# Kernel optimization log

Hardware: AMD Instinct MI355X
Metric: run time of the kernel (lower is better)

## Reference

```python
import jax, jax.numpy as jnp
import numpy as np

D_MODEL = 2048
N_HEADS = 16
D_HEAD = 128
N_GROUPS = 4          # KV heads = N_HEADS // N_GROUPS = 4
D_FF = 2048           # hard-coded default in FeedForward
EPS = 1e-6


def setup_inputs() -> dict:
    key = jax.random.key(0)
    ks = jax.random.split(key, 16)
    B, S = 4, 1024
    Hkv = N_HEADS // N_GROUPS
    s = 0.02
    inp = {
        "x": jax.random.normal(ks[0], (B, S, D_MODEL), jnp.float32),
        "scale1": jnp.ones((D_MODEL,), jnp.float32),
        "Wq": jax.random.normal(ks[1], (D_MODEL, N_HEADS * D_HEAD), jnp.float32) * s,
        "bq": jnp.zeros((N_HEADS * D_HEAD,), jnp.float32),
        "Wk": jax.random.normal(ks[2], (D_MODEL, Hkv * D_HEAD), jnp.float32) * s,
        "bk": jnp.zeros((Hkv * D_HEAD,), jnp.float32),
        "Wv": jax.random.normal(ks[3], (D_MODEL, Hkv * D_HEAD), jnp.float32) * s,
        "bv": jnp.zeros((Hkv * D_HEAD,), jnp.float32),
        "Wo": jax.random.normal(ks[4], (N_HEADS * D_HEAD, D_MODEL), jnp.float32) * s,
        "bo": jnp.zeros((D_MODEL,), jnp.float32),
        "W1": jax.random.normal(ks[5], (D_MODEL, D_FF), jnp.float32) * s,
        "b1": jnp.zeros((D_FF,), jnp.float32),
        "W2": jax.random.normal(ks[6], (D_FF, D_MODEL), jnp.float32) * s,
        "b2": jnp.zeros((D_MODEL,), jnp.float32),
    }
    return inp


def _rmsnorm(x, scale):
    rms = jnp.sqrt(jnp.mean(x * x, axis=-1, keepdims=True) + EPS)
    return scale * (x / rms)


def reference(x, scale1, Wq, bq, Wk, bk, Wv, bv, Wo, bo, W1, b1, W2, b2):
    B, S, _ = x.shape
    Hkv = N_HEADS // N_GROUPS
    xn = _rmsnorm(x, scale1)  # [B,S,D]

    # GQA attention (prefill, step=None -> no cache)
    Q = (xn @ Wq + bq).reshape(B, S, N_HEADS, D_HEAD).transpose(0, 2, 1, 3)  # [B,H,S,d]
    K = (xn @ Wk + bk).reshape(B, S, Hkv, D_HEAD).transpose(0, 2, 1, 3)      # [B,Hkv,S,d]
    V = (xn @ Wv + bv).reshape(B, S, Hkv, D_HEAD).transpose(0, 2, 1, 3)
    Kr = jnp.repeat(K, N_GROUPS, axis=1)  # [B,H,S,d]
    Vr = jnp.repeat(V, N_GROUPS, axis=1)
    scores = jnp.einsum("bhqd,bhkd->bhqk", Q, Kr) / jnp.sqrt(jnp.float32(D_HEAD))
    attn = jax.nn.softmax(scores, axis=-1)
    out = jnp.einsum("bhqk,bhkd->bhqd", attn, Vr)  # [B,H,S,d]
    out = out.transpose(0, 2, 1, 3).reshape(B, S, N_HEADS * D_HEAD)
    x = x + out @ Wo + bo

    # Source bug preserved: FFN consumes rms_norm1 output, rms_norm2 is dead code
    h = xn @ W1 + b1
    h = h * jax.nn.sigmoid(h) * h  # x_ff * silu(x_ff)
    x = x + h @ W2 + b2
    return x
```

## Files before the change

kernel.cpp:

```cpp
#include <hip/hip_runtime.h>
#include <hip/hip_bf16.h>
#include <cstdint>

using bf16 = __hip_bfloat16;
typedef __attribute__((ext_vector_type(8))) __bf16 bf16x8;
typedef __attribute__((ext_vector_type(4))) float f32x4;

#define MFMA16(a, b, c) __builtin_amdgcn_mfma_f32_16x16x32_bf16((a), (b), (c), 0, 0, 0)

#if __has_builtin(__builtin_amdgcn_exp2f)
__device__ __forceinline__ float fexp2(float x) { return __builtin_amdgcn_exp2f(x); }
#else
__device__ __forceinline__ float fexp2(float x) { return exp2f(x); }
#endif

__device__ __forceinline__ void async16(void* lds_ptr, const void* gptr) {
  auto g = reinterpret_cast<__attribute__((address_space(1))) unsigned int*>(
      reinterpret_cast<uintptr_t>(gptr));
  auto l = reinterpret_cast<__attribute__((address_space(3))) unsigned int*>(
      static_cast<unsigned int>(reinterpret_cast<uintptr_t>(lds_ptr)));
  __builtin_amdgcn_global_load_lds(g, l, 16, 0, 0);
}

__global__ __launch_bounds__(256) void rmsnorm_cast_k(
    const float* __restrict__ x, const float* __restrict__ sc, bf16* __restrict__ xn) {
  const int row = blockIdx.x, tid = threadIdx.x;
  const float4* xr = (const float4*)(x + (size_t)row * 2048);
  float4 a = xr[tid * 2], b = xr[tid * 2 + 1];
  float ss = a.x * a.x + a.y * a.y + a.z * a.z + a.w * a.w +
             b.x * b.x + b.y * b.y + b.z * b.z + b.w * b.w;
#pragma unroll
  for (int d = 1; d < 64; d <<= 1) ss += __shfl_xor(ss, d);
  __shared__ float sm[4];
  if ((tid & 63) == 0) sm[tid >> 6] = ss;
  __syncthreads();
  const float rinv = rsqrtf((sm[0] + sm[1] + sm[2] + sm[3]) * (1.0f / 2048.0f) + 1e-6f);
  const float4* sp = (const float4*)sc;
  float4 s0 = sp[tid * 2], s1 = sp[tid * 2 + 1];
  union { bf16 h[8]; bf16x8 v; } o;
  o.h[0] = __float2bfloat16(a.x * rinv * s0.x);
  o.h[1] = __float2bfloat16(a.y * rinv * s0.y);
  o.h[2] = __float2bfloat16(a.z * rinv * s0.z);
  o.h[3] = __float2bfloat16(a.w * rinv * s0.w);
  o.h[4] = __float2bfloat16(b.x * rinv * s1.x);
  o.h[5] = __float2bfloat16(b.y * rinv * s1.y);
  o.h[6] = __float2bfloat16(b.z * rinv * s1.z);
  o.h[7] = __float2bfloat16(b.w * rinv * s1.w);
  *(bf16x8*)(xn + (size_t)row * 2048 + tid * 8) = o.v;
}

__global__ void transpose_cast_k(const float* __restrict__ W, bf16* __restrict__ Wt,
                                 int N, int row_off) {
  __shared__ float t[32][33];
  const int n0 = blockIdx.x * 32, k0 = blockIdx.y * 32;
  const int tx = threadIdx.x, ty = threadIdx.y;
#pragma unroll
  for (int i = 0; i < 4; ++i)
    t[ty + 8 * i][tx] = W[(size_t)(k0 + ty + 8 * i) * N + n0 + tx];
  __syncthreads();
#pragma unroll
  for (int i = 0; i < 4; ++i)
    Wt[(size_t)(row_off + n0 + ty + 8 * i) * 2048 + k0 + tx] =
        __float2bfloat16(t[tx][ty + 8 * i]);
}

__global__ void transpose_v_k(const bf16* __restrict__ qkv, bf16* __restrict__ vtb) {
  __shared__ bf16 t[32][33];
  const int bh = blockIdx.z, b = bh >> 2, g = bh & 3;
  const int s0 = blockIdx.x * 32, d0 = blockIdx.y * 32;
  const int tx = threadIdx.x, ty = threadIdx.y;
#pragma unroll
  for (int i = 0; i < 4; ++i)
    t[ty + 8 * i][tx] =
        qkv[(size_t)(b * 1024 + s0 + ty + 8 * i) * 3072 + 2560 + g * 128 + d0 + tx];
  __syncthreads();
#pragma unroll
  for (int i = 0; i < 4; ++i)
    vtb[((size_t)bh * 128 + d0 + ty + 8 * i) * 1024 + s0 + tx] = t[tx][ty + 8 * i];
}

__global__ void concat_bias_k(const float* __restrict__ bq, const float* __restrict__ bk,
                              const float* __restrict__ bv, const float* __restrict__ b1,
                              float* __restrict__ o) {
  const int i = blockIdx.x * 256 + threadIdx.x;
  if (i < 2048) o[i] = bq[i];
  else if (i < 2560) o[i] = bk[i - 2048];
  else if (i < 3072) o[i] = bv[i - 2560];
  else o[i] = b1[i - 3072];
}

#define GR_PHASE(HH, DO_STAGE, VMW)                                                \
  {                                                                                \
    const int sa = ((HH) & 3) * 8192, sb = 32768 + sa;                             \
    bf16x8 af[4], bf_[4];                                                          \
    _Pragma("unroll") for (int mi = 0; mi < 4; ++mi) {                             \
      const int R = (w >> 1) * 64 + mi * 16 + lo;                                  \
      af[mi] = *(const bf16x8*)(lds + sa + R * 64 + ((hi ^ ((R >> 1) & 3)) << 4)); \
    }                                                                              \
    _Pragma("unroll") for (int nj = 0; nj < 4; ++nj) {                             \
      const int S = (w & 1) * 64 + nj * 16 + lo;                                   \
      bf_[nj] = *(const bf16x8*)(lds + sb + S * 64 + ((hi ^ ((S >> 1) & 3)) << 4)); \
    }                                                                              \
    DO_STAGE;                                                                      \
    asm volatile("s_waitcnt vmcnt(" #VMW ")" ::: "memory");                        \
    __builtin_amdgcn_sched_barrier(0);                                             \
    __builtin_amdgcn_s_barrier();                                                  \
    asm volatile("" ::: "memory");                                                 \
    __builtin_amdgcn_s_setprio(1);                                                 \
    _Pragma("unroll") for (int mi = 0; mi < 4; ++mi)                               \
      _Pragma("unroll") for (int nj = 0; nj < 4; ++nj)                             \
        acc[mi][nj] = MFMA16(af[mi], bf_[nj], acc[mi][nj]);                        \
    __builtin_amdgcn_s_setprio(0);                                                 \
    asm volatile("" ::: "memory");                                                 \
    __builtin_amdgcn_s_barrier();                                                  \
    asm volatile("" ::: "memory");                                                 \
  }

template <int EPI>
__global__ __launch_bounds__(256, 2) void gemm_r(
    const bf16* __restrict__ A, const bf16* __restrict__ Bt,
    const float* __restrict__ bias, const float* __restrict__ res,
    void* __restrict__ out0, void* __restrict__ out1, int K) {
  __shared__ __align__(16) unsigned char lds[65536];
  const int tid = threadIdx.x, lane = tid & 63, w = tid >> 6;
  const int hi = lane >> 4, lo = lane & 15;
  const int brow = blockIdx.x * 128, bcol = blockIdx.y * 128;
  const int nt = K >> 6;

  const int o0 = tid * 16, o1 = o0 + 4096;
  const int r0 = o0 >> 6, c0 = ((((o0 >> 4) & 3) ^ ((r0 >> 1) & 3)) << 3);
  const int r1 = o1 >> 6, c1 = ((((o1 >> 4) & 3) ^ ((r1 >> 1) & 3)) << 3);
  const bf16* gA0 = A + (size_t)(brow + r0) * K + c0;
  const bf16* gA1 = A + (size_t)(brow + r1) * K + c1;
  const bf16* gB0 = Bt + (size_t)(bcol + r0) * K + c0;
  const bf16* gB1 = Bt + (size_t)(bcol + r1) * K + c1;

  auto stg = [&](int h) {
    const int s = (h & 3) * 8192;
    const int kb = h * 32;
    async16(lds + s + o0, gA0 + kb);
    async16(lds + s + o1, gA1 + kb);
    async16(lds + 32768 + s + o0, gB0 + kb);
    async16(lds + 32768 + s + o1, gB1 + kb);
  };

  stg(0); stg(1); stg(2);
  asm volatile("s_waitcnt vmcnt(8)" ::: "memory");
  __builtin_amdgcn_sched_barrier(0);
  __builtin_amdgcn_s_barrier();
  asm volatile("" ::: "memory");

  f32x4 acc[4][4] = {};
  int t = 0;
  for (; t < nt - 2; ++t) {
    GR_PHASE(2 * t,     stg(2 * t + 3), 8);
    GR_PHASE(2 * t + 1, stg(2 * t + 4), 8);
  }
  GR_PHASE(2 * t,     stg(2 * t + 3), 8);
  GR_PHASE(2 * t + 1, (void)0, 4);
  ++t;
  GR_PHASE(2 * t,     (void)0, 0);
  GR_PHASE(2 * t + 1, (void)0, 0);

#pragma unroll
  for (int nj = 0; nj < 4; ++nj) {
    const int col = bcol + (w & 1) * 64 + nj * 16 + lo;
    const float bs = bias[col];
#pragma unroll
    for (int mi = 0; mi < 4; ++mi) {
      const int row0 = brow + (w >> 1) * 64 + mi * 16 + hi * 4;
#pragma unroll
      for (int r = 0; r < 4; ++r) {
        float v = acc[mi][nj][r] + bs;
        const int row = row0 + r;
        if (EPI == 0) {
          if (bcol < 3072) {
            ((bf16*)out0)[(size_t)row * 3072 + col] = __float2bfloat16(v);
          } else {
            const float sg = 1.0f / (1.0f + __expf(-v));
            v = v * sg * v;
            ((bf16*)out1)[(size_t)row * 2048 + (col - 3072)] = __float2bfloat16(v);
          }
        } else {
          v += res[(size_t)row * 2048 + col];
          ((float*)out0)[(size_t)row * 2048 + col] = v;
        }
      }
    }
  }
}

__global__ __launch_bounds__(256, 4) void attn_fwd(
    const bf16* __restrict__ qkv, const bf16* __restrict__ vtb, bf16* __restrict__ out) {
  __shared__ __align__(16) unsigned char lds[40960];
  unsigned char* Ks = lds;
  unsigned char* Vs = lds + 16384;
  unsigned char* Ps = lds + 32768;
  const int tid = threadIdx.x, lane = tid & 63, w = tid >> 6;
  const int hi = lane >> 4, lo = lane & 15;
  const int qt = blockIdx.x, bh = blockIdx.y;
  const int b = bh >> 4, h = bh & 15, g = h >> 2;
  const size_t tok0 = (size_t)b * 1024;
  const int q0 = qt * 64;

  bf16x8 qf[4];
  {
    const bf16* qp = qkv + (tok0 + q0 + w * 16 + lo) * 3072 + h * 128 + hi * 8;
#pragma unroll
    for (int kc = 0; kc < 4; ++kc) qf[kc] = *(const bf16x8*)(qp + kc * 32);
  }

  float m2 = -1e30f, lsum = 0.f;
  f32x4 oacc[8] = {};
  const float c2 = 0.08838834764831845f * 1.44269504088896f;

  const int o = tid * 16;
  const bf16* kbase = qkv + tok0 * 3072 + 2048 + g * 128;
  const bf16* vbase = vtb + (size_t)(b * 4 + g) * 128 * 1024;
  unsigned char* Pw = Ps + w * 2048;

  for (int t = 0; t < 16; ++t) {
    const int kb = t * 64;
#pragma unroll
    for (int rd = 0; rd < 4; ++rd) {
      const int oo = o + rd * 4096;
      const int rK = oo >> 8, cK = ((oo >> 4) & 15) ^ (rK & 15);
      const int rV = oo >> 7, cV = ((oo >> 4) & 7) ^ (rV & 7);
      async16(Ks + oo, kbase + (size_t)(kb + rK) * 3072 + cK * 8);
      async16(Vs + oo, vbase + (size_t)rV * 1024 + kb + cV * 8);
    }
    __syncthreads();

    f32x4 sc[4] = {};
#pragma unroll
    for (int kc = 0; kc < 4; ++kc) {
#pragma unroll
      for (int kg = 0; kg < 4; ++kg) {
        const int row = kg * 16 + lo;
        bf16x8 kf = *(const bf16x8*)(Ks + row * 256 + ((((kc << 2) + hi) ^ (row & 15)) << 4));
        sc[kg] = MFMA16(kf, qf[kc], sc[kg]);
      }
    }

    float mx = sc[0][0];
#pragma unroll
    for (int kg = 0; kg < 4; ++kg)
#pragma unroll
      for (int r = 0; r < 4; ++r) mx = fmaxf(mx, sc[kg][r]);
    mx = fmaxf(mx, __shfl_xor(mx, 16));
    mx = fmaxf(mx, __shfl_xor(mx, 32));
    mx *= c2;
    const float mn = fmaxf(m2, mx);
    const float corr = fexp2(m2 - mn);
    m2 = mn;

    float rs = 0.f;
#pragma unroll
    for (int kg = 0; kg < 4; ++kg) {
      union { bf16 hh[4]; uint2 v; } pk;
#pragma unroll
      for (int r = 0; r < 4; ++r) {
        const float p = fexp2(sc[kg][r] * c2 - mn);
        rs += p;
        pk.hh[r] = __float2bfloat16(p);
      }
      *(uint2*)(Pw + lo * 128 + ((((kg << 1) + (hi >> 1)) ^ (lo & 7)) << 4) +
                ((hi & 1) << 3)) = pk.v;
    }
    rs += __shfl_xor(rs, 16);
    rs += __shfl_xor(rs, 32);
    lsum = lsum * corr + rs;

    float corr_r[4];
#pragma unroll
    for (int r = 0; r < 4; ++r) corr_r[r] = __shfl(corr, hi * 4 + r);
#pragma unroll
    for (int dg = 0; dg < 8; ++dg)
#pragma unroll
      for (int r = 0; r < 4; ++r) oacc[dg][r] *= corr_r[r];

    asm volatile("s_waitcnt lgkmcnt(0)" ::: "memory");

    bf16x8 pf[2];
#pragma unroll
    for (int kc = 0; kc < 2; ++kc)
      pf[kc] = *(const bf16x8*)(Pw + lo * 128 + ((((kc << 2) + hi) ^ (lo & 7)) << 4));
#pragma unroll
    for (int dg = 0; dg < 8; ++dg) {
#pragma unroll
      for (int kc = 0; kc < 2; ++kc) {
        const int vrow = dg * 16 + lo;
        bf16x8 vf = *(const bf16x8*)(Vs + vrow * 128 + ((((kc << 2) + hi) ^ (vrow & 7)) << 4));
        oacc[dg] = MFMA16(pf[kc], vf, oacc[dg]);
      }
    }
    __syncthreads();
  }

  const float linv = 1.0f / lsum;
  float lr[4];
#pragma unroll
  for (int r = 0; r < 4; ++r) lr[r] = __shfl(linv, hi * 4 + r);
  bf16* op = out + (tok0 + q0 + w * 16 + hi * 4) * 2048 + h * 128 + lo;
#pragma unroll
  for (int dg = 0; dg < 8; ++dg)
#pragma unroll
    for (int r = 0; r < 4; ++r)
      op[(size_t)r * 2048 + dg * 16] = __float2bfloat16(oacc[dg][r] * lr[r]);
}

extern "C" void kernel_launch(void* const* d_in, const int* in_sizes, int n_in,
                              void* d_out, int out_size, void* d_ws, size_t ws_size,
                              hipStream_t stream) {
  (void)in_sizes; (void)n_in; (void)out_size; (void)ws_size;
  const float* x  = (const float*)d_in[0];
  const float* s1 = (const float*)d_in[1];
  const float* Wq = (const float*)d_in[2];
  const float* bq = (const float*)d_in[3];
  const float* Wk = (const float*)d_in[4];
  const float* bk = (const float*)d_in[5];
  const float* Wv = (const float*)d_in[6];
  const float* bv = (const float*)d_in[7];
  const float* Wo = (const float*)d_in[8];
  const float* bo = (const float*)d_in[9];
  const float* W1 = (const float*)d_in[10];
  const float* b1 = (const float*)d_in[11];
  const float* W2 = (const float*)d_in[12];
  const float* b2 = (const float*)d_in[13];
  float* outp = (float*)d_out;

  char* ws = (char*)d_ws;
  bf16*  xn    = (bf16*)(ws + 0);
  bf16*  vtb   = (bf16*)(ws + 0);
  bf16*  wcatT = (bf16*)(ws + 16777216);
  bf16*  attnb = (bf16*)(ws + 16777216);
  float* bcat  = (float*)(ws + 37748736);
  bf16*  woT   = (bf16*)(ws + 37769216);
  bf16*  w2T   = (bf16*)(ws + 46157824);
  bf16*  qkvb  = (bf16*)(ws + 54546432);
  bf16*  gbuf  = (bf16*)(ws + 79712256);
  float* x1    = outp;

  const dim3 b32x8(32, 8);
  rmsnorm_cast_k<<<dim3(4096), dim3(256), 0, stream>>>(x, s1, xn);
  concat_bias_k<<<dim3(20), dim3(256), 0, stream>>>(bq, bk, bv, b1, bcat);
  transpose_cast_k<<<dim3(64, 64), b32x8, 0, stream>>>(Wq, wcatT, 2048, 0);
  transpose_cast_k<<<dim3(16, 64), b32x8, 0, stream>>>(Wk, wcatT, 512, 2048);
  transpose_cast_k<<<dim3(16, 64), b32x8, 0, stream>>>(Wv, wcatT, 512, 2560);
  transpose_cast_k<<<dim3(64, 64), b32x8, 0, stream>>>(W1, wcatT, 2048, 3072);
  transpose_cast_k<<<dim3(64, 64), b32x8, 0, stream>>>(Wo, woT, 2048, 0);
  transpose_cast_k<<<dim3(64, 64), b32x8, 0, stream>>>(W2, w2T, 2048, 0);
  gemm_r<0><<<dim3(32, 40), dim3(256), 0, stream>>>(xn, wcatT, bcat, (const float*)nullptr,
                                                    (void*)qkvb, (void*)gbuf, 2048);
  transpose_v_k<<<dim3(32, 4, 16), b32x8, 0, stream>>>(qkvb, vtb);
  attn_fwd<<<dim3(16, 64), dim3(256), 0, stream>>>(qkvb, vtb, attnb);
  gemm_r<1><<<dim3(32, 16), dim3(256), 0, stream>>>(attnb, woT, bo, x, (void*)x1,
                                                    (void*)nullptr, 2048);
  gemm_r<1><<<dim3(32, 16), dim3(256), 0, stream>>>(gbuf, w2T, b2, x1, (void*)outp,
                                                    (void*)nullptr, 2048);
}
```

Baseline: 284.4 us.

## Double-buffer LDS fragment reads and cut barriers in GEMM main loop

Restructures the GEMM inner loop so the LDS fragments for the next half-tile are read into a second register set while the current one feeds the MFMAs. This drops one of the two s_barriers per phase and deepens the global-load wait so stages are kept further ahead. It adds 32 extra VGPRs of fragment storage, which may strain occupancy at launch bound 2, and depends on subtle synchronisation correctness across the 4-slot ring.

Result: no change. 287.2 us (+1.0%).

```diff
diff --git a/kernel.cpp b/kernel.cpp
--- a/kernel.cpp
+++ b/kernel.cpp
@@ -89,32 +89,31 @@
   else o[i] = b1[i - 3072];
 }
 
-#define GR_PHASE(HH, DO_STAGE, VMW)                                                \
+#define PH_READ(AF, BF, SLOT)                                                      \
   {                                                                                \
-    const int sa = ((HH) & 3) * 8192, sb = 32768 + sa;                             \
-    bf16x8 af[4], bf_[4];                                                          \
+    const int sa = (SLOT)*8192, sb = 32768 + sa;                                   \
     _Pragma("unroll") for (int mi = 0; mi < 4; ++mi) {                             \
       const int R = (w >> 1) * 64 + mi * 16 + lo;                                  \
-      af[mi] = *(const bf16x8*)(lds + sa + R * 64 + ((hi ^ ((R >> 1) & 3)) << 4)); \
+      AF[mi] = *(const bf16x8*)(lds + sa + R * 64 + ((hi ^ ((R >> 1) & 3)) << 4)); \
     }                                                                              \
     _Pragma("unroll") for (int nj = 0; nj < 4; ++nj) {                             \
       const int S = (w & 1) * 64 + nj * 16 + lo;                                   \
-      bf_[nj] = *(const bf16x8*)(lds + sb + S * 64 + ((hi ^ ((S >> 1) & 3)) << 4)); \
+      BF[nj] = *(const bf16x8*)(lds + sb + S * 64 + ((hi ^ ((S >> 1) & 3)) << 4)); \
     }                                                                              \
-    DO_STAGE;                                                                      \
-    asm volatile("s_waitcnt vmcnt(" #VMW ")" ::: "memory");                        \
-    __builtin_amdgcn_sched_barrier(0);                                             \
-    __builtin_amdgcn_s_barrier();                                                  \
-    asm volatile("" ::: "memory");                                                 \
-    __builtin_amdgcn_s_setprio(1);                                                 \
-    _Pragma("unroll") for (int mi = 0; mi < 4; ++mi)                               \
-      _Pragma("unroll") for (int nj = 0; nj < 4; ++nj)                             \
-        acc[mi][nj] = MFMA16(af[mi], bf_[nj], acc[mi][nj]);                        \
-    __builtin_amdgcn_s_setprio(0);                                                 \
-    asm volatile("" ::: "memory");                                                 \
-    __builtin_amdgcn_s_barrier();                                                  \
-    asm volatile("" ::: "memory");                                                 \
-  }
+  }
+
+#define PH_MFMA(AF, BF)                                                            \
+  __builtin_amdgcn_s_setprio(1);                                                   \
+  _Pragma("unroll") for (int mi = 0; mi < 4; ++mi)                                 \
+    _Pragma("unroll") for (int nj = 0; nj < 4; ++nj)                               \
+      acc[mi][nj] = MFMA16(AF[mi], BF[nj], acc[mi][nj]);                           \
+  __builtin_amdgcn_s_setprio(0);
+
+#define PH_TAIL_SYNC                                                               \
+  asm volatile("s_waitcnt lgkmcnt(0)" ::: "memory");                               \
+  __builtin_amdgcn_sched_barrier(0);                                               \
+  __builtin_amdgcn_s_barrier();                                                    \
+  asm volatile("" ::: "memory");
 
 template <int EPI>
 __global__ __launch_bounds__(256, 2) void gemm_r(
@@ -145,22 +144,47 @@
   };
 
   stg(0); stg(1); stg(2);
-  asm volatile("s_waitcnt vmcnt(8)" ::: "memory");
+  asm volatile("s_waitcnt vmcnt(4)" ::: "memory");
   __builtin_amdgcn_sched_barrier(0);
   __builtin_amdgcn_s_barrier();
   asm volatile("" ::: "memory");
 
   f32x4 acc[4][4] = {};
-  int t = 0;
-  for (; t < nt - 2; ++t) {
-    GR_PHASE(2 * t,     stg(2 * t + 3), 8);
-    GR_PHASE(2 * t + 1, stg(2 * t + 4), 8);
-  }
-  GR_PHASE(2 * t,     stg(2 * t + 3), 8);
-  GR_PHASE(2 * t + 1, (void)0, 4);
-  ++t;
-  GR_PHASE(2 * t,     (void)0, 0);
-  GR_PHASE(2 * t + 1, (void)0, 0);
+  bf16x8 afA[4], bfA[4], afB[4], bfB[4];
+  PH_READ(afA, bfA, 0);
+
+  for (int t = 0; t < nt - 2; ++t) {
+    const int h = 2 * t;
+    PH_READ(afB, bfB, (h + 1) & 3);
+    stg(h + 3);
+    asm volatile("s_waitcnt vmcnt(4)" ::: "memory");
+    __builtin_amdgcn_sched_barrier(0);
+    PH_MFMA(afA, bfA);
+    PH_TAIL_SYNC;
+    PH_READ(afA, bfA, (h + 2) & 3);
+    stg(h + 4);
+    asm volatile("s_waitcnt vmcnt(4)" ::: "memory");
+    __builtin_amdgcn_sched_barrier(0);
+    PH_MFMA(afB, bfB);
+    PH_TAIL_SYNC;
+  }
+  {
+    const int ht = 2 * nt - 4;
+    PH_READ(afB, bfB, (ht + 1) & 3);
+    stg(ht + 3);
+    asm volatile("s_waitcnt vmcnt(4)" ::: "memory");
+    __builtin_amdgcn_sched_barrier(0);
+    PH_MFMA(afA, bfA);
+    PH_TAIL_SYNC;
+    PH_READ(afA, bfA, (ht + 2) & 3);
+    asm volatile("s_waitcnt vmcnt(0)" ::: "memory");
+    __builtin_amdgcn_sched_barrier(0);
+    PH_MFMA(afB, bfB);
+    PH_TAIL_SYNC;
+    PH_READ(afB, bfB, (ht + 3) & 3);
+    PH_MFMA(afA, bfA);
+    PH_MFMA(afB, bfB);
+  }
 
 #pragma unroll
   for (int nj = 0; nj < 4; ++nj) {
```
